# Kernel optimization log

Measured on AMD Instinct MI355X. Metric: run time of the kernel, lower is better.

The kernel has to match this reference:

```python
import jax, jax.numpy as jnp
import numpy as np

B, N = 4096, 64
HID, NHEAD, NLAYERS, OUT = 128, 4, 2, 1
LIDAR, PROC = 20, 20
FOV = 0.35 * np.pi
MAXD = 10.0
LN_EPS = 1e-5


def _lin(x, W, b):
    # torch.nn.Linear: y = x @ W.T + b, W is [out, in]
    return x @ W.T + b


def _ln(x, g, b):
    m = jnp.mean(x, -1, keepdims=True)
    v = jnp.var(x, -1, keepdims=True)  # population variance, as torch LayerNorm
    return (x - m) / jnp.sqrt(v + LN_EPS) * g + b


def _adj_mask(pos):
    # pos: [B,N,2]. Edge i -> j exists where final_mask[b,i,j] (src=i, dst=j).
    dx = pos[:, :, 0][:, :, None] - pos[:, :, 0][:, None, :]  # x_i - x_j
    dy = pos[:, :, 1][:, :, None] - pos[:, :, 1][:, None, :]
    dist = jnp.sqrt(dx * dx + dy * dy)
    ang = jnp.arctan2(dy, dx)
    ang = (ang + np.pi) % (2 * np.pi) - np.pi
    eye = jnp.eye(pos.shape[1], dtype=bool)
    return (~eye)[None] & (jnp.abs(ang) <= FOV) & (dist <= MAXD)


def _forward(data, W_l1, b_l1, W_l2, b_l2, W11, b11, W12, b12, W21, b21, W22, b22,
             Wqkv, bqkv, Wo, bo, ln1_g, ln1_b, Wf1, bf1, Wf2, bf2, ln2_g, ln2_b, Wfc, bfc):
    orig, lidar = data[..., :7], data[..., 7:]
    lf = jax.nn.relu(_lin(jax.nn.relu(_lin(lidar, W_l1, b_l1)), W_l2, b_l2))
    x = jnp.concatenate([orig, lf], -1)  # [B,N,PROC+7]
    # graph construction is index/mask logic -> no gradient through it
    m = jax.lax.stop_gradient(_adj_mask(x[..., :2])).astype(x.dtype)  # [B,N,N]
    # GINConv (eps=0): h_j = nn(x_j + sum_{i: i->j} x_i)
    aggr = jnp.einsum('bij,bif->bjf', m, x)
    h = jax.nn.relu(_lin(jax.nn.relu(_lin(x + aggr, W11, b11)), W12, b12))
    aggr = jnp.einsum('bij,bif->bjf', m, h)
    h = jax.nn.relu(_lin(jax.nn.relu(_lin(h + aggr, W21, b21)), W22, b22))
    # TransformerEncoder over x.unsqueeze(1): seq_len == 1 per node, so the
    # softmax over a single key is exactly 1 -> attn(x) = out_proj(v_proj(x)).
    t = h.reshape(B * N, HID)
    for l in range(NLAYERS):
        Wv, bv = Wqkv[l][2 * HID:], bqkv[l][2 * HID:]
        attn = _lin(_lin(t, Wv, bv), Wo[l], bo[l])
        t = _ln(t + attn, ln1_g[l], ln1_b[l])
        ff = _lin(jax.nn.relu(_lin(t, Wf1[l], bf1[l])), Wf2[l], bf2[l])
        t = _ln(t + ff, ln2_g[l], ln2_b[l])
    return _lin(t.reshape(B, N, HID), Wfc, bfc)  # [B,N,OUT]


def setup_inputs():
    key = jax.random.key(0)
    ks = iter(jax.random.split(key, 40))
    def p(shape, s=0.05):
        return jax.random.normal(next(ks), shape, jnp.float32) * s
    return dict(
        data=jax.random.normal(next(ks), (B, N, 7 + LIDAR), jnp.float32),
        W_l1=p((HID, LIDAR)), b_l1=p((HID,)),
        W_l2=p((PROC, HID)), b_l2=p((PROC,)),
        W11=p((HID, PROC + 7)), b11=p((HID,)),
        W12=p((HID, HID)), b12=p((HID,)),
        W21=p((HID, HID)), b21=p((HID,)),
        W22=p((HID, HID)), b22=p((HID,)),
        Wqkv=p((NLAYERS, 3 * HID, HID)), bqkv=p((NLAYERS, 3 * HID)),
        Wo=p((NLAYERS, HID, HID)), bo=p((NLAYERS, HID)),
        ln1_g=jnp.ones((NLAYERS, HID), jnp.float32), ln1_b=jnp.zeros((NLAYERS, HID), jnp.float32),
        Wf1=p((NLAYERS, HID, HID)), bf1=p((NLAYERS, HID)),
        Wf2=p((NLAYERS, HID, HID)), bf2=p((NLAYERS, HID)),
        ln2_g=jnp.ones((NLAYERS, HID), jnp.float32), ln2_b=jnp.zeros((NLAYERS, HID), jnp.float32),
        Wfc=p((OUT, HID)), bfc=p((OUT,)),
    )


def reference(data, W_l1, b_l1, W_l2, b_l2, W11, b11, W12, b12, W21, b21, W22, b22,
              Wqkv, bqkv, Wo, bo, ln1_g, ln1_b, Wf1, bf1, Wf2, bf2, ln2_g, ln2_b, Wfc, bfc):
    return _forward(data, W_l1, b_l1, W_l2, b_l2, W11, b11, W12, b12, W21, b21, W22, b22,
                    Wqkv, bqkv, Wo, bo, ln1_g, ln1_b, Wf1, bf1, Wf2, bf2, ln2_g, ln2_b, Wfc, bfc)
```

## Files before the change

kernel.cpp:

```cpp
#include <hip/hip_runtime.h>
#include <math.h>

#define NB 4096
#define NN 64

typedef _Float16 h8 __attribute__((ext_vector_type(8)));
typedef _Float16 h4 __attribute__((ext_vector_type(4)));
typedef float f4 __attribute__((ext_vector_type(4)));
typedef unsigned long long u64;

typedef const __attribute__((address_space(1))) void* gas_t;
typedef __attribute__((address_space(3))) void* las_t;

__device__ __forceinline__ void gload16(const void* g, void* l) {
  __builtin_amdgcn_global_load_lds((gas_t)g, (las_t)l, 16, 0, 0);
}
__device__ __forceinline__ void rbar() {
  asm volatile("" ::: "memory");
  __builtin_amdgcn_s_barrier();
  asm volatile("" ::: "memory");
}
__device__ __forceinline__ void lgkm0() {
  asm volatile("s_waitcnt lgkmcnt(0)" ::: "memory");
}
template<int N> __device__ __forceinline__ void waitv() {
  if constexpr (N == 0) asm volatile("s_waitcnt vmcnt(0)" ::: "memory");
  else                  asm volatile("s_waitcnt vmcnt(1)" ::: "memory");
  __builtin_amdgcn_sched_barrier(0);
}

__device__ __forceinline__ int aoff(int row, int colb) {
  return row * 256 + (colb ^ ((row & 7) << 4));
}
__device__ __forceinline__ h8 ald8(const char* a, int row, int colb) {
  return *(const h8*)(a + aoff(row, colb));
}
__device__ __forceinline__ void ast8(char* a, int row, int colb, h8 v) {
  *(h8*)(a + aoff(row, colb)) = v;
}
__device__ __forceinline__ _Float16 ald(const char* a, int row, int colb) {
  return *(const _Float16*)(a + aoff(row, colb));
}
__device__ __forceinline__ void ast(char* a, int row, int colb, _Float16 v) {
  *(_Float16*)(a + aoff(row, colb)) = v;
}

__global__ void prepA(
    const float* __restrict__ W_l1, const float* __restrict__ W_l2,
    const float* __restrict__ W11, const float* __restrict__ W12,
    const float* __restrict__ W21, const float* __restrict__ W22,
    const float* __restrict__ Wf1, const float* __restrict__ Wf2,
    const float* __restrict__ b_l1, const float* __restrict__ b_l2,
    const float* __restrict__ b11, const float* __restrict__ b12,
    const float* __restrict__ b21, const float* __restrict__ b22,
    const float* __restrict__ bf1, const float* __restrict__ bf2,
    const float* __restrict__ ln1_g, const float* __restrict__ ln1_b,
    const float* __restrict__ ln2_g, const float* __restrict__ ln2_b,
    _Float16* __restrict__ ws)
{
  const int e = blockIdx.x * 256 + threadIdx.x;
  float v;
  if (e < 4096) { const int o = e >> 5, k = e & 31; v = (k < 20) ? W_l1[o * 20 + k] : 0.f; }
  else if (e < 8192) { const int i = e - 4096; const int o = i >> 7, k = i & 127; v = (o < 20) ? W_l2[o * 128 + k] : 0.f; }
  else if (e < 12288) { const int i = e - 8192; const int o = i >> 5, k = i & 31; v = (k < 27) ? W11[o * 27 + k] : 0.f; }
  else if (e < 28672) v = W12[e - 12288];
  else if (e < 45056) v = W21[e - 28672];
  else if (e < 61440) v = W22[e - 45056];
  else if (e < 94208) return;
  else if (e < 126976) v = Wf1[e - 94208];
  else if (e < 159744) v = Wf2[e - 126976];
  else {
    const int p = e - 159744;
    if (p >= 2560) return;
    const int idx = p >> 7, col = p & 127;
    switch (idx) {
      case 0: v = b_l1[col]; break;
      case 1: v = (col < 20) ? b_l2[col] : 0.f; break;
      case 2: v = b11[col]; break;
      case 3: v = b12[col]; break;
      case 4: v = b21[col]; break;
      case 5: v = b22[col]; break;
      case 8: v = bf1[col]; break;
      case 9: v = bf2[col]; break;
      case 10: v = bf1[128 + col]; break;
      case 11: v = bf2[128 + col]; break;
      case 12: v = ln1_g[col]; break;
      case 13: v = ln1_b[col]; break;
      case 14: v = ln2_g[col]; break;
      case 15: v = ln2_b[col]; break;
      case 16: v = ln1_g[128 + col]; break;
      case 17: v = ln1_b[128 + col]; break;
      case 18: v = ln2_g[128 + col]; break;
      case 19: v = ln2_b[128 + col]; break;
      default: v = 0.f; break;
    }
  }
  ws[e] = (_Float16)v;
}

__global__ void prepB(
    const float* __restrict__ Wqkv, const float* __restrict__ bqkv,
    const float* __restrict__ Wo, const float* __restrict__ bo,
    _Float16* __restrict__ ws)
{
  if (blockIdx.x < 128) {
    const int e = blockIdx.x * 256 + threadIdx.x;
    const int l = e >> 14, r = e & 16383, o = r >> 7, k = r & 127;
    const float* wo = Wo + (l * 128 + o) * 128;
    const float* wv = Wqkv + l * 49152 + 32768 + k;
    float acc = 0.f;
#pragma unroll 4
    for (int m = 0; m < 128; ++m) acc += wo[m] * wv[m * 128];
    ws[61440 + e] = (_Float16)acc;
  } else {
    const int t = threadIdx.x;
    const int l = t >> 7, o = t & 127;
    const float* wo = Wo + (l * 128 + o) * 128;
    const float* bv = bqkv + l * 384 + 256;
    float acc = bo[l * 128 + o];
    for (int m = 0; m < 128; ++m) acc += bv[m] * wo[m];
    ws[159744 + (6 + l) * 128 + o] = (_Float16)acc;
  }
}

__device__ __forceinline__ void stage64(const _Float16* __restrict__ Wp, int KT,
                                        int kc, int oc, char* buf, int tid) {
  const int o = tid >> 2, kq = tid & 3;
  const int kreal = kq ^ ((o >> 1) & 3);
  gload16(Wp + (oc * 64 + o) * KT + kc * 32 + kreal * 8, buf + tid * 16);
}
__device__ __forceinline__ void stage32(const _Float16* __restrict__ Wp,
                                        int kc, char* buf, int tid) {
  const int o = tid >> 3, u = tid & 7;
  const int ureal = u ^ (o & 7);
  gload16(Wp + o * 128 + kc * 64 + ureal * 8, buf + tid * 16);
}

struct Cap { h4 q0[8]; h4 q1[8]; };

template<int EPI, bool CAP, bool LAST, typename PF>
__device__ __forceinline__ Cap mm128_stage(
    const _Float16* __restrict__ Wp, char* g0, char* g1,
    const _Float16* pb, int bidx, Cap rin,
    char* wbase, int q0, int tid, PF&& pf)
{
  const int lane = tid & 63, wv = tid >> 6, lc = lane & 15, kg = lane >> 4;
  const int nrow = wv * 16 + lc;

  h8 bf0[4], bf1[4];
#pragma unroll
  for (int i = 0; i < 4; ++i) {
    bf0[i] = ald8(g0, nrow, i * 64 + kg * 16);
    bf1[i] = ald8(g1, nrow, i * 64 + kg * 16);
  }
  Cap rout{};
#pragma unroll
  for (int oc = 0; oc < 2; ++oc) {
    f4 a0[4], a1[4];
#pragma unroll
    for (int t = 0; t < 4; ++t) { a0[t] = (f4){0.f,0.f,0.f,0.f}; a1[t] = (f4){0.f,0.f,0.f,0.f}; }
#pragma unroll
    for (int kc = 0; kc < 4; ++kc) {
      const int ql = oc * 4 + kc;
      if (LAST && ql == 7) waitv<0>(); else waitv<1>();
      rbar();
      const int s = ql + 2;
      char* nbuf = wbase + ((q0 + s) % 3) * 4096;
      if (s < 8) stage64(Wp, 128, s & 3, s >> 2, nbuf, tid);
      else pf(s - 8, nbuf);
      const char* wb = wbase + ((q0 + ql) % 3) * 4096;
#pragma unroll
      for (int t = 0; t < 4; ++t) {
        const int o = t * 16 + lc;
        const int kq = kg ^ ((o >> 1) & 3);
        const h8 af = *(const h8*)(wb + (o * 4 + kq) * 16);
        a0[t] = __builtin_amdgcn_mfma_f32_16x16x32_f16(af, bf0[kc], a0[t], 0, 0, 0);
        a1[t] = __builtin_amdgcn_mfma_f32_16x16x32_f16(af, bf1[kc], a1[t], 0, 0, 0);
      }
    }
#pragma unroll
    for (int t = 0; t < 4; ++t) {
      const int slot = oc * 4 + t;
      const int fb = slot * 16 + kg * 4;
      const int cb = fb * 2;
      h4 bq{};
      if constexpr (EPI != 1) bq = *(const h4*)(pb + bidx * 128 + fb);
      h4 r0q{}, r1q{};
      if constexpr (EPI == 2) {
        r0q = *(const h4*)(g0 + aoff(nrow, cb));
        r1q = *(const h4*)(g1 + aoff(nrow, cb));
      }
      if constexpr (CAP) {
        rout.q0[slot] = *(const h4*)(g0 + aoff(nrow, cb));
        rout.q1[slot] = *(const h4*)(g1 + aoff(nrow, cb));
      }
      h4 o0, o1;
#pragma unroll
      for (int r = 0; r < 4; ++r) {
        float v0 = a0[t][r], v1 = a1[t][r];
        if constexpr (EPI != 1) { v0 += (float)bq[r]; v1 += (float)bq[r]; }
        if constexpr (EPI == 2) { v0 += (float)r0q[r]; v1 += (float)r1q[r]; }
        if constexpr (EPI == 3) { v0 += (float)rin.q0[slot][r]; v1 += (float)rin.q1[slot][r]; }
        if constexpr (EPI == 0) { v0 = fmaxf(v0, 0.f); v1 = fmaxf(v1, 0.f); }
        o0[r] = (_Float16)v0; o1[r] = (_Float16)v1;
      }
      *(h4*)(g0 + aoff(nrow, cb)) = o0;
      *(h4*)(g1 + aoff(nrow, cb)) = o1;
    }
  }
  return rout;
}

template<typename PF>
__device__ __forceinline__ void mm32z_stage(
    const _Float16* __restrict__ Wp, char* g0, char* g1,
    char* wbase, int q0, int tid, PF&& pf)
{
  const int lane = tid & 63, wv = tid >> 6, lc = lane & 15, kg = lane >> 4;
  const int nrow = wv * 16 + lc;
  const h8 bf0 = ald8(g0, nrow, 64 + kg * 16);
  const h8 bf1 = ald8(g1, nrow, 64 + kg * 16);
#pragma unroll
  for (int oc = 0; oc < 2; ++oc) {
    waitv<1>(); rbar();
    pf(oc, wbase + ((q0 + oc + 2) % 3) * 4096);
    const char* wb = wbase + ((q0 + oc) % 3) * 4096;
    f4 a0[4], a1[4];
#pragma unroll
    for (int t = 0; t < 4; ++t) { a0[t] = (f4){0.f,0.f,0.f,0.f}; a1[t] = (f4){0.f,0.f,0.f,0.f}; }
#pragma unroll
    for (int t = 0; t < 4; ++t) {
      const int o = t * 16 + lc;
      const int kq = kg ^ ((o >> 1) & 3);
      const h8 af = *(const h8*)(wb + (o * 4 + kq) * 16);
      a0[t] = __builtin_amdgcn_mfma_f32_16x16x32_f16(af, bf0, a0[t], 0, 0, 0);
      a1[t] = __builtin_amdgcn_mfma_f32_16x16x32_f16(af, bf1, a1[t], 0, 0, 0);
    }
#pragma unroll
    for (int t = 0; t < 4; ++t) {
      const int fb = (oc * 4 + t) * 16 + kg * 4;
      const int cb = fb * 2;
      h4 o0, o1;
#pragma unroll
      for (int r = 0; r < 4; ++r) { o0[r] = (_Float16)a0[t][r]; o1[r] = (_Float16)a1[t][r]; }
      *(h4*)(g0 + aoff(nrow, cb)) = o0;
      *(h4*)(g1 + aoff(nrow, cb)) = o1;
    }
  }
}

__device__ __forceinline__ void agg_ip(const u64* mc, char* G, const _Float16* pb,
                                       int bidx, int tid)
{
  const int lane = tid & 63, wv = tid >> 6, lc = lane & 15, kg = lane >> 4;
  const int c0 = wv * 32 + lc;
  u64 mrow[4];
#pragma unroll
  for (int rt = 0; rt < 4; ++rt) mrow[rt] = mc[rt * 16 + lc];
  h8 bf[2][2];
#pragma unroll
  for (int ks = 0; ks < 2; ++ks)
#pragma unroll
    for (int ct = 0; ct < 2; ++ct)
#pragma unroll
      for (int e = 0; e < 8; ++e)
        bf[ks][ct][e] = ald(G, ks * 32 + kg * 8 + e, (c0 + ct * 16) * 2);
  lgkm0(); rbar();
  f4 acc[4][2];
#pragma unroll
  for (int rt = 0; rt < 4; ++rt) { acc[rt][0] = (f4){0.f,0.f,0.f,0.f}; acc[rt][1] = (f4){0.f,0.f,0.f,0.f}; }
#pragma unroll
  for (int ks = 0; ks < 2; ++ks)
#pragma unroll
    for (int rt = 0; rt < 4; ++rt) {
      const unsigned int byte = (unsigned int)(mrow[rt] >> (ks * 32 + kg * 8)) & 0xffu;
      h8 af;
#pragma unroll
      for (int e = 0; e < 8; ++e) af[e] = (_Float16)((byte >> e) & 1u);
#pragma unroll
      for (int ct = 0; ct < 2; ++ct)
        acc[rt][ct] = __builtin_amdgcn_mfma_f32_16x16x32_f16(af, bf[ks][ct], acc[rt][ct], 0, 0, 0);
    }
#pragma unroll
  for (int ct = 0; ct < 2; ++ct) {
    const int col = c0 + ct * 16;
    const float bv = (float)pb[bidx * 128 + col];
#pragma unroll
    for (int rt = 0; rt < 4; ++rt)
#pragma unroll
      for (int qq = 0; qq < 4; ++qq)
        ast(G, rt * 16 + kg * 4 + qq, col * 2, (_Float16)fmaxf(acc[rt][ct][qq] + bv, 0.f));
  }
}

__device__ __forceinline__ void layer_norm(char* buf, const _Float16* pb, int lnidx, int tid)
{
  const int n = tid >> 2, q = tid & 3;
  float vals[32];
#pragma unroll
  for (int u = 0; u < 4; ++u) {
    const h8 v = ald8(buf, n, q * 64 + u * 16);
#pragma unroll
    for (int e = 0; e < 8; ++e) vals[u * 8 + e] = (float)v[e];
  }
  float s = 0.f;
#pragma unroll
  for (int u = 0; u < 32; ++u) s += vals[u];
  s += __shfl_xor(s, 1, 64);
  s += __shfl_xor(s, 2, 64);
  const float mean = s * 0.0078125f;
  float vv = 0.f;
#pragma unroll
  for (int u = 0; u < 32; ++u) { const float d = vals[u] - mean; vv = fmaf(d, d, vv); }
  vv += __shfl_xor(vv, 1, 64);
  vv += __shfl_xor(vv, 2, 64);
  const float rstd = 1.0f / sqrtf(vv * 0.0078125f + 1e-5f);
#pragma unroll
  for (int u = 0; u < 4; ++u) {
    h8 o;
#pragma unroll
    for (int e = 0; e < 8; ++e) {
      const int col = q * 32 + u * 8 + e;
      const float gg = (float)pb[lnidx * 128 + col];
      const float bb = (float)pb[(lnidx + 1) * 128 + col];
      o[e] = (_Float16)((vals[u * 8 + e] - mean) * rstd * gg + bb);
    }
    ast8(buf, n, q * 64 + u * 16, o);
  }
}

struct SM {
  alignas(16) char G0[16384];
  alignas(16) char G1[16384];
  alignas(16) char WB[12288];
  alignas(16) char PB[5120];
  u64 mcol[2][64];
};

__global__ __launch_bounds__(256, 2)
void gin_critic_kernel(
    const float* __restrict__ data,
    const float* __restrict__ Wfc, const float* __restrict__ bfc,
    const _Float16* __restrict__ ws,
    float* __restrict__ out)
{
  __shared__ SM sm;
  const int tid = threadIdx.x;
  const int lane = tid & 63, wv = tid >> 6, lc = lane & 15, kg = lane >> 4;
  const int row0 = wv * 16 + lc, rb = wv * 16 + kg * 4;
  const int b = blockIdx.x;
  const long base = (long)b * 2 * NN * 27;
  char* G0 = sm.G0; char* G1 = sm.G1; char* wbase = sm.WB;
  const _Float16* pb = (const _Float16*)sm.PB;

  const _Float16* Wl1p = ws + 0;
  const _Float16* Wl2p = ws + 4096;
  const _Float16* W11p = ws + 8192;
  const _Float16* W12p = ws + 12288;
  const _Float16* W21p = ws + 28672;
  const _Float16* W22p = ws + 45056;
  const _Float16* Wat0 = ws + 61440;
  const _Float16* Wat1 = ws + 61440 + 16384;
  const _Float16* Wf1_0 = ws + 94208;
  const _Float16* Wf1_1 = ws + 94208 + 16384;
  const _Float16* Wf2_0 = ws + 126976;
  const _Float16* Wf2_1 = ws + 126976 + 16384;

#pragma unroll
  for (int i = 0; i < 14; ++i) {
    const int idx = tid + i * 256;
    const int cidx = idx < 3456 ? idx : 3455;
    float v = data[base + cidx];
    asm volatile("" : "+v"(v));
    if (idx < 3456) {
      const int gi = idx / 1728;
      const int r = idx - gi * 1728;
      const int n = r / 27, f = r - n * 27;
      char* Gg = gi ? G1 : G0;
      if (f < 7) ast(Gg, n, 64 + f * 2, (_Float16)v);
      else       ast(Gg, n, (f - 7) * 2, (_Float16)v);
    }
  }
  if (tid < 128) {
    const int gi = tid >> 6, n = tid & 63;
    char* Gg = gi ? G1 : G0;
#pragma unroll
    for (int c = 20; c < 32; ++c) ast(Gg, n, c * 2, (_Float16)0.f);
#pragma unroll
    for (int c = 59; c < 64; ++c) ast(Gg, n, c * 2, (_Float16)0.f);
  }
  const float* pp = data + base + (long)(wv >> 1) * 1728 + lane * 27;
  const float px = pp[0], py = pp[1];
  lgkm0(); rbar();

  {
    const int g = wv >> 1;
    const float FOVF = (float)(0.35 * 3.14159265358979323846);
    const double TT = tan(0.35 * 3.14159265358979323846);
    const double T2 = TT * TT;
    for (int jj = 0; jj < 32; ++jj) {
      const int j = (wv & 1) * 32 + jj;
      const float x0j = __shfl(px, j, 64);
      const float x1j = __shfl(py, j, 64);
      const float dxf = px - x0j;
      const float dyf = py - x1j;
      const float dist = sqrtf(dxf * dxf + dyf * dyf);
      bool pred;
      if (lane == j || dist > 10.0f) {
        pred = false;
      } else if (dxf <= 0.0f) {
        pred = (dxf == 0.0f && dyf == 0.0f);
      } else {
        const double qa = (double)dyf * (double)dyf;
        const double qb = (double)dxf * (double)dxf * T2;
        if (qa <= qb * 0.99999) pred = true;
        else if (qa >= qb * 1.00001) pred = false;
        else pred = (fabsf((float)atan2((double)dyf, (double)dxf)) <= FOVF);
      }
      const u64 bal = __ballot(pred);
      if (lane == 0) sm.mcol[g][j] = bal | (1ull << j);
    }
  }

  gload16(ws + 159744 + (size_t)tid * 8, sm.PB + (size_t)tid * 16);
  gload16(ws + 159744 + 2048 + (size_t)(tid & 63) * 8, sm.PB + 4096 + (size_t)(tid & 63) * 16);
  stage64(Wl1p, 32, 0, 0, wbase + 0 * 4096, tid);
  stage32(Wl2p, 0, wbase + 1 * 4096, tid);

  h8 axl0, axl1;
  f4 l20[2], l21[2];
  l20[0] = l20[1] = l21[0] = l21[1] = (f4){0.f,0.f,0.f,0.f};
  waitv<1>(); rbar();
  stage64(Wl1p, 32, 0, 1, wbase + 2 * 4096, tid);
  axl0 = ald8(G0, row0, kg * 16);
  axl1 = ald8(G1, row0, kg * 16);
  {
    const char* wb = wbase + 0 * 4096;
    f4 a0[4], a1[4];
#pragma unroll
    for (int t = 0; t < 4; ++t) { a0[t] = (f4){0.f,0.f,0.f,0.f}; a1[t] = (f4){0.f,0.f,0.f,0.f}; }
#pragma unroll
    for (int t = 0; t < 4; ++t) {
      const int o = t * 16 + lc;
      const int kq = kg ^ ((o >> 1) & 3);
      const h8 bf = *(const h8*)(wb + (o * 4 + kq) * 16);
      a0[t] = __builtin_amdgcn_mfma_f32_16x16x32_f16(axl0, bf, a0[t], 0, 0, 0);
      a1[t] = __builtin_amdgcn_mfma_f32_16x16x32_f16(axl1, bf, a1[t], 0, 0, 0);
    }
#pragma unroll
    for (int t = 0; t < 4; ++t) {
      const int col = t * 16 + lc;
      const float bv = (float)pb[0 * 128 + col];
#pragma unroll
      for (int r = 0; r < 4; ++r) {
        ast(G0, rb + r, 128 + col * 2, (_Float16)fmaxf(a0[t][r] + bv, 0.f));
        ast(G1, rb + r, 128 + col * 2, (_Float16)fmaxf(a1[t][r] + bv, 0.f));
      }
    }
  }
  waitv<1>(); rbar();
  stage32(Wl2p, 1, wbase + 0 * 4096, tid);
  {
    const char* wb = wbase + 1 * 4096;
    h8 ah0[2], ah1[2];
#pragma unroll
    for (int i = 0; i < 2; ++i) {
      ah0[i] = ald8(G0, row0, 128 + i * 64 + kg * 16);
      ah1[i] = ald8(G1, row0, 128 + i * 64 + kg * 16);
    }
#pragma unroll
    for (int ks = 0; ks < 2; ++ks)
#pragma unroll
      for (int ct = 0; ct < 2; ++ct) {
        const int o = ct * 16 + lc;
        const int u = (ks * 4 + kg) ^ (o & 7);
        const h8 bf = *(const h8*)(wb + (o * 8 + u) * 16);
        l20[ct] = __builtin_amdgcn_mfma_f32_16x16x32_f16(ah0[ks], bf, l20[ct], 0, 0, 0);
        l21[ct] = __builtin_amdgcn_mfma_f32_16x16x32_f16(ah1[ks], bf, l21[ct], 0, 0, 0);
      }
  }
  waitv<1>(); rbar();
  stage64(W11p, 32, 0, 0, wbase + 1 * 4096, tid);
  {
    const char* wb = wbase + 2 * 4096;
    f4 a0[4], a1[4];
#pragma unroll
    for (int t = 0; t < 4; ++t) { a0[t] = (f4){0.f,0.f,0.f,0.f}; a1[t] = (f4){0.f,0.f,0.f,0.f}; }
#pragma unroll
    for (int t = 0; t < 4; ++t) {
      const int o = t * 16 + lc;
      const int kq = kg ^ ((o >> 1) & 3);
      const h8 bf = *(const h8*)(wb + (o * 4 + kq) * 16);
      a0[t] = __builtin_amdgcn_mfma_f32_16x16x32_f16(axl0, bf, a0[t], 0, 0, 0);
      a1[t] = __builtin_amdgcn_mfma_f32_16x16x32_f16(axl1, bf, a1[t], 0, 0, 0);
    }
#pragma unroll
    for (int t = 0; t < 4; ++t) {
      const int col = t * 16 + lc;
      const float bv = (float)pb[0 * 128 + 64 + col];
#pragma unroll
      for (int r = 0; r < 4; ++r) {
        ast(G0, rb + r, 128 + col * 2, (_Float16)fmaxf(a0[t][r] + bv, 0.f));
        ast(G1, rb + r, 128 + col * 2, (_Float16)fmaxf(a1[t][r] + bv, 0.f));
      }
    }
  }
  waitv<1>(); rbar();
  stage64(W11p, 32, 0, 1, wbase + 2 * 4096, tid);
  {
    const char* wb = wbase + 0 * 4096;
    h8 ah0[2], ah1[2];
#pragma unroll
    for (int i = 0; i < 2; ++i) {
      ah0[i] = ald8(G0, row0, 128 + i * 64 + kg * 16);
      ah1[i] = ald8(G1, row0, 128 + i * 64 + kg * 16);
    }
#pragma unroll
    for (int ks = 0; ks < 2; ++ks)
#pragma unroll
      for (int ct = 0; ct < 2; ++ct) {
        const int o = ct * 16 + lc;
        const int u = (ks * 4 + kg) ^ (o & 7);
        const h8 bf = *(const h8*)(wb + (o * 8 + u) * 16);
        l20[ct] = __builtin_amdgcn_mfma_f32_16x16x32_f16(ah0[ks], bf, l20[ct], 0, 0, 0);
        l21[ct] = __builtin_amdgcn_mfma_f32_16x16x32_f16(ah1[ks], bf, l21[ct], 0, 0, 0);
      }
#pragma unroll
    for (int ct = 0; ct < 2; ++ct) {
      const int col = ct * 16 + lc;
      if (col < 20) {
        const float bv = (float)pb[1 * 128 + col];
#pragma unroll
        for (int r = 0; r < 4; ++r) {
          ast(G0, rb + r, 78 + col * 2, (_Float16)fmaxf(l20[ct][r] + bv, 0.f));
          ast(G1, rb + r, 78 + col * 2, (_Float16)fmaxf(l21[ct][r] + bv, 0.f));
        }
      }
    }
  }

  Cap rz{};
  mm32z_stage(W11p, G0, G1, wbase, 4, tid,
      [&](int s, char* buf) { stage64(W12p, 128, s, 0, buf, tid); });
  lgkm0(); rbar();
  agg_ip(sm.mcol[0], G0, pb, 2, tid);
  agg_ip(sm.mcol[1], G1, pb, 2, tid);
  lgkm0(); rbar();
  mm128_stage<0, false, false>(W12p, G0, G1, pb, 3, rz, wbase, 6, tid,
      [&](int s, char* buf) { stage64(W21p, 128, s, 0, buf, tid); });
  mm128_stage<1, false, false>(W21p, G0, G1, pb, 0, rz, wbase, 14, tid,
      [&](int s, char* buf) { stage64(W22p, 128, s, 0, buf, tid); });
  lgkm0(); rbar();
  agg_ip(sm.mcol[0], G0, pb, 4, tid);
  agg_ip(sm.mcol[1], G1, pb, 4, tid);
  lgkm0(); rbar();
  mm128_stage<0, false, false>(W22p, G0, G1, pb, 5, rz, wbase, 22, tid,
      [&](int s, char* buf) { stage64(Wat0, 128, s, 0, buf, tid); });
  mm128_stage<2, false, false>(Wat0, G0, G1, pb, 6, rz, wbase, 30, tid,
      [&](int s, char* buf) { stage64(Wf1_0, 128, s, 0, buf, tid); });
  layer_norm(G0, pb, 12, tid);
  layer_norm(G1, pb, 12, tid);
  Cap c0 = mm128_stage<0, true, false>(Wf1_0, G0, G1, pb, 8, rz, wbase, 38, tid,
      [&](int s, char* buf) { stage64(Wf2_0, 128, s, 0, buf, tid); });
  mm128_stage<3, false, false>(Wf2_0, G0, G1, pb, 9, c0, wbase, 46, tid,
      [&](int s, char* buf) { stage64(Wat1, 128, s, 0, buf, tid); });
  layer_norm(G0, pb, 14, tid);
  layer_norm(G1, pb, 14, tid);
  mm128_stage<2, false, false>(Wat1, G0, G1, pb, 7, rz, wbase, 54, tid,
      [&](int s, char* buf) { stage64(Wf1_1, 128, s, 0, buf, tid); });
  layer_norm(G0, pb, 16, tid);
  layer_norm(G1, pb, 16, tid);
  Cap c1 = mm128_stage<0, true, false>(Wf1_1, G0, G1, pb, 10, rz, wbase, 62, tid,
      [&](int s, char* buf) { stage64(Wf2_1, 128, s, 0, buf, tid); });
  mm128_stage<3, false, true>(Wf2_1, G0, G1, pb, 11, c1, wbase, 70, tid,
      [&](int, char*) {});
  layer_norm(G0, pb, 18, tid);
  layer_norm(G1, pb, 18, tid);

#pragma unroll
  for (int g = 0; g < 2; ++g) {
    const char* Pg = g ? G1 : G0;
    const int n = tid >> 2, q = tid & 3;
    float s = 0.f;
#pragma unroll
    for (int u = 0; u < 4; ++u) {
      const h8 v = ald8(Pg, n, q * 64 + u * 16);
      const float4 w0 = *(const float4*)(Wfc + q * 32 + u * 8);
      const float4 w1 = *(const float4*)(Wfc + q * 32 + u * 8 + 4);
      s = fmaf((float)v[0], w0.x, s); s = fmaf((float)v[1], w0.y, s);
      s = fmaf((float)v[2], w0.z, s); s = fmaf((float)v[3], w0.w, s);
      s = fmaf((float)v[4], w1.x, s); s = fmaf((float)v[5], w1.y, s);
      s = fmaf((float)v[6], w1.z, s); s = fmaf((float)v[7], w1.w, s);
    }
    s += __shfl_xor(s, 1, 64);
    s += __shfl_xor(s, 2, 64);
    if (q == 0) out[((long)b * 2 + g) * NN + n] = s + bfc[0];
  }
}

extern "C" void kernel_launch(void* const* d_in, const int* in_sizes, int n_in,
                              void* d_out, int out_size, void* d_ws, size_t ws_size,
                              hipStream_t stream) {
  const float* data  = (const float*)d_in[0];
  const float* W_l1  = (const float*)d_in[1];
  const float* b_l1  = (const float*)d_in[2];
  const float* W_l2  = (const float*)d_in[3];
  const float* b_l2  = (const float*)d_in[4];
  const float* W11   = (const float*)d_in[5];
  const float* b11   = (const float*)d_in[6];
  const float* W12   = (const float*)d_in[7];
  const float* b12   = (const float*)d_in[8];
  const float* W21   = (const float*)d_in[9];
  const float* b21   = (const float*)d_in[10];
  const float* W22   = (const float*)d_in[11];
  const float* b22   = (const float*)d_in[12];
  const float* Wqkv  = (const float*)d_in[13];
  const float* bqkv  = (const float*)d_in[14];
  const float* Wo    = (const float*)d_in[15];
  const float* bo    = (const float*)d_in[16];
  const float* ln1_g = (const float*)d_in[17];
  const float* ln1_b = (const float*)d_in[18];
  const float* Wf1   = (const float*)d_in[19];
  const float* bf1   = (const float*)d_in[20];
  const float* Wf2   = (const float*)d_in[21];
  const float* bf2   = (const float*)d_in[22];
  const float* ln2_g = (const float*)d_in[23];
  const float* ln2_b = (const float*)d_in[24];
  const float* Wfc   = (const float*)d_in[25];
  const float* bfc   = (const float*)d_in[26];

  _Float16* ws = (_Float16*)d_ws;

  prepA<<<dim3(634), dim3(256), 0, stream>>>(
      W_l1, W_l2, W11, W12, W21, W22, Wf1, Wf2,
      b_l1, b_l2, b11, b12, b21, b22, bf1, bf2,
      ln1_g, ln1_b, ln2_g, ln2_b, ws);
  prepB<<<dim3(129), dim3(256), 0, stream>>>(Wqkv, bqkv, Wo, bo, ws);

  gin_critic_kernel<<<dim3(NB / 2), dim3(256), 0, stream>>>(
      data, Wfc, bfc, ws, (float*)d_out);
}
```

Before: 198.8 us.

## Store pre-aggregation GEMM output transposed so adjacency aggregation reads contiguous fragments

```diff
diff --git a/kernel.cpp b/kernel.cpp
--- a/kernel.cpp
+++ b/kernel.cpp
@@ -30,7 +30,7 @@
 }
 
 __device__ __forceinline__ int aoff(int row, int colb) {
-  return row * 256 + (colb ^ ((row & 7) << 4));
+  return row * 256 + (colb ^ ((row & 15) << 4));
 }
 __device__ __forceinline__ h8 ald8(const char* a, int row, int colb) {
   return *(const h8*)(a + aoff(row, colb));
@@ -43,6 +43,9 @@
 }
 __device__ __forceinline__ void ast(char* a, int row, int colb, _Float16 v) {
   *(_Float16*)(a + aoff(row, colb)) = v;
+}
+__device__ __forceinline__ int zoff(int f, int nb) {
+  return f * 128 + ((((nb >> 4) ^ (f & 7)) << 4) | (nb & 15));
 }
 
 __global__ void prepA(
@@ -198,7 +201,7 @@
 #pragma unroll
       for (int r = 0; r < 4; ++r) {
         float v0 = a0[t][r], v1 = a1[t][r];
-        if constexpr (EPI != 1) { v0 += (float)bq[r]; v1 += (float)bq[r]; }
+        v0 += (float)bq[r]; v1 += (float)bq[r];
         if constexpr (EPI == 2) { v0 += (float)r0q[r]; v1 += (float)r1q[r]; }
         if constexpr (EPI == 3) { v0 += (float)rin.q0[slot][r]; v1 += (float)rin.q1[slot][r]; }
         if constexpr (EPI == 0) { v0 = fmaxf(v0, 0.f); v1 = fmaxf(v1, 0.f); }
@@ -212,14 +215,14 @@
 }
 
 template<typename PF>
-__device__ __forceinline__ void mm32z_stage(
+__device__ __forceinline__ void mm32z_old(
     const _Float16* __restrict__ Wp, char* g0, char* g1,
     char* wbase, int q0, int tid, PF&& pf)
 {
   const int lane = tid & 63, wv = tid >> 6, lc = lane & 15, kg = lane >> 4;
-  const int nrow = wv * 16 + lc;
-  const h8 bf0 = ald8(g0, nrow, 64 + kg * 16);
-  const h8 bf1 = ald8(g1, nrow, 64 + kg * 16);
+  const int row0 = wv * 16 + lc, rb = wv * 16 + kg * 4;
+  const h8 af0 = ald8(g0, row0, 64 + kg * 16);
+  const h8 af1 = ald8(g1, row0, 64 + kg * 16);
 #pragma unroll
   for (int oc = 0; oc < 2; ++oc) {
     waitv<1>(); rbar();
@@ -232,64 +235,126 @@
     for (int t = 0; t < 4; ++t) {
       const int o = t * 16 + lc;
       const int kq = kg ^ ((o >> 1) & 3);
-      const h8 af = *(const h8*)(wb + (o * 4 + kq) * 16);
-      a0[t] = __builtin_amdgcn_mfma_f32_16x16x32_f16(af, bf0, a0[t], 0, 0, 0);
-      a1[t] = __builtin_amdgcn_mfma_f32_16x16x32_f16(af, bf1, a1[t], 0, 0, 0);
+      const h8 wf = *(const h8*)(wb + (o * 4 + kq) * 16);
+      a0[t] = __builtin_amdgcn_mfma_f32_16x16x32_f16(af0, wf, a0[t], 0, 0, 0);
+      a1[t] = __builtin_amdgcn_mfma_f32_16x16x32_f16(af1, wf, a1[t], 0, 0, 0);
     }
 #pragma unroll
     for (int t = 0; t < 4; ++t) {
-      const int fb = (oc * 4 + t) * 16 + kg * 4;
-      const int cb = fb * 2;
+      const int o = oc * 64 + t * 16 + lc;
       h4 o0, o1;
 #pragma unroll
       for (int r = 0; r < 4; ++r) { o0[r] = (_Float16)a0[t][r]; o1[r] = (_Float16)a1[t][r]; }
-      *(h4*)(g0 + aoff(nrow, cb)) = o0;
-      *(h4*)(g1 + aoff(nrow, cb)) = o1;
-    }
-  }
-}
-
-__device__ __forceinline__ void agg_ip(const u64* mc, char* G, const _Float16* pb,
-                                       int bidx, int tid)
+      *(h4*)(g0 + zoff(o, rb * 2)) = o0;
+      *(h4*)(g1 + zoff(o, rb * 2)) = o1;
+    }
+  }
+}
+
+template<typename PF>
+__device__ __forceinline__ void mm128z_old(
+    const _Float16* __restrict__ Wp, char* g0, char* g1,
+    char* wbase, int q0, int tid, PF&& pf)
 {
   const int lane = tid & 63, wv = tid >> 6, lc = lane & 15, kg = lane >> 4;
-  const int c0 = wv * 32 + lc;
-  u64 mrow[4];
-#pragma unroll
-  for (int rt = 0; rt < 4; ++rt) mrow[rt] = mc[rt * 16 + lc];
-  h8 bf[2][2];
+  const int row0 = wv * 16 + lc, rb = wv * 16 + kg * 4;
+  h8 af0[4], af1[4];
+#pragma unroll
+  for (int i = 0; i < 4; ++i) {
+    af0[i] = ald8(g0, row0, i * 64 + kg * 16);
+    af1[i] = ald8(g1, row0, i * 64 + kg * 16);
+  }
+#pragma unroll
+  for (int oc = 0; oc < 2; ++oc) {
+    f4 a0[4], a1[4];
+#pragma unroll
+    for (int t = 0; t < 4; ++t) { a0[t] = (f4){0.f,0.f,0.f,0.f}; a1[t] = (f4){0.f,0.f,0.f,0.f}; }
+#pragma unroll
+    for (int kc = 0; kc < 4; ++kc) {
+      const int ql = oc * 4 + kc;
+      waitv<1>();
+      rbar();
+      const int s = ql + 2;
+      char* nbuf = wbase + ((q0 + s) % 3) * 4096;
+      if (s < 8) stage64(Wp, 128, s & 3, s >> 2, nbuf, tid);
+      else pf(s - 8, nbuf);
+      const char* wb = wbase + ((q0 + ql) % 3) * 4096;
+#pragma unroll
+      for (int t = 0; t < 4; ++t) {
+        const int o = t * 16 + lc;
+        const int kq = kg ^ ((o >> 1) & 3);
+        const h8 wf = *(const h8*)(wb + (o * 4 + kq) * 16);
+        a0[t] = __builtin_amdgcn_mfma_f32_16x16x32_f16(af0[kc], wf, a0[t], 0, 0, 0);
+        a1[t] = __builtin_amdgcn_mfma_f32_16x16x32_f16(af1[kc], wf, a1[t], 0, 0, 0);
+      }
+    }
+#pragma unroll
+    for (int t = 0; t < 4; ++t) {
+      const int o = oc * 64 + t * 16 + lc;
+      h4 o0, o1;
+#pragma unroll
+      for (int r = 0; r < 4; ++r) { o0[r] = (_Float16)a0[t][r]; o1[r] = (_Float16)a1[t][r]; }
+      *(h4*)(g0 + zoff(o, rb * 2)) = o0;
+      *(h4*)(g1 + zoff(o, rb * 2)) = o1;
+    }
+  }
+}
+
+__device__ __forceinline__ void agg2_zt(
+    const u64* mc0, const u64* mc1, char* g0, char* g1,
+    const _Float16* pb, int bidx, int tid)
+{
+  const int lane = tid & 63, wv = tid >> 6, lc = lane & 15, kg = lane >> 4;
+  const int fb = wv * 32;
+  h8 a0[2][2], a1[2][2];
+#pragma unroll
+  for (int mt = 0; mt < 2; ++mt)
+#pragma unroll
+    for (int ks = 0; ks < 2; ++ks) {
+      a0[mt][ks] = *(const h8*)(g0 + zoff(fb + mt * 16 + lc, ks * 64 + kg * 16));
+      a1[mt][ks] = *(const h8*)(g1 + zoff(fb + mt * 16 + lc, ks * 64 + kg * 16));
+    }
+  u64 mr0[4], mr1[4];
+#pragma unroll
+  for (int nt = 0; nt < 4; ++nt) { mr0[nt] = mc0[nt * 16 + lc]; mr1[nt] = mc1[nt * 16 + lc]; }
+  lgkm0(); rbar();
+  f4 c0[2][4], c1[2][4];
+#pragma unroll
+  for (int mt = 0; mt < 2; ++mt)
+#pragma unroll
+    for (int nt = 0; nt < 4; ++nt) { c0[mt][nt] = (f4){0.f,0.f,0.f,0.f}; c1[mt][nt] = (f4){0.f,0.f,0.f,0.f}; }
 #pragma unroll
   for (int ks = 0; ks < 2; ++ks)
 #pragma unroll
-    for (int ct = 0; ct < 2; ++ct)
-#pragma unroll
-      for (int e = 0; e < 8; ++e)
-        bf[ks][ct][e] = ald(G, ks * 32 + kg * 8 + e, (c0 + ct * 16) * 2);
-  lgkm0(); rbar();
-  f4 acc[4][2];
-#pragma unroll
-  for (int rt = 0; rt < 4; ++rt) { acc[rt][0] = (f4){0.f,0.f,0.f,0.f}; acc[rt][1] = (f4){0.f,0.f,0.f,0.f}; }
-#pragma unroll
-  for (int ks = 0; ks < 2; ++ks)
-#pragma unroll
-    for (int rt = 0; rt < 4; ++rt) {
-      const unsigned int byte = (unsigned int)(mrow[rt] >> (ks * 32 + kg * 8)) & 0xffu;
-      h8 af;
-#pragma unroll
-      for (int e = 0; e < 8; ++e) af[e] = (_Float16)((byte >> e) & 1u);
-#pragma unroll
-      for (int ct = 0; ct < 2; ++ct)
-        acc[rt][ct] = __builtin_amdgcn_mfma_f32_16x16x32_f16(af, bf[ks][ct], acc[rt][ct], 0, 0, 0);
-    }
-#pragma unroll
-  for (int ct = 0; ct < 2; ++ct) {
-    const int col = c0 + ct * 16;
-    const float bv = (float)pb[bidx * 128 + col];
-#pragma unroll
-    for (int rt = 0; rt < 4; ++rt)
-#pragma unroll
-      for (int qq = 0; qq < 4; ++qq)
-        ast(G, rt * 16 + kg * 4 + qq, col * 2, (_Float16)fmaxf(acc[rt][ct][qq] + bv, 0.f));
+    for (int nt = 0; nt < 4; ++nt) {
+      h8 b0, b1;
+#pragma unroll
+      for (int e = 0; e < 8; ++e) {
+        b0[e] = (_Float16)((mr0[nt] >> (ks * 32 + kg * 8 + e)) & 1ull);
+        b1[e] = (_Float16)((mr1[nt] >> (ks * 32 + kg * 8 + e)) & 1ull);
+      }
+#pragma unroll
+      for (int mt = 0; mt < 2; ++mt) {
+        c0[mt][nt] = __builtin_amdgcn_mfma_f32_16x16x32_f16(a0[mt][ks], b0, c0[mt][nt], 0, 0, 0);
+        c1[mt][nt] = __builtin_amdgcn_mfma_f32_16x16x32_f16(a1[mt][ks], b1, c1[mt][nt], 0, 0, 0);
+      }
+    }
+#pragma unroll
+  for (int mt = 0; mt < 2; ++mt) {
+    const int f0 = fb + mt * 16 + kg * 4;
+    const h4 bq = *(const h4*)(pb + bidx * 128 + f0);
+#pragma unroll
+    for (int nt = 0; nt < 4; ++nt) {
+      const int j = nt * 16 + lc;
+      h4 o0, o1;
+#pragma unroll
+      for (int r = 0; r < 4; ++r) {
+        o0[r] = (_Float16)fmaxf(c0[mt][nt][r] + (float)bq[r], 0.f);
+        o1[r] = (_Float16)fmaxf(c1[mt][nt][r] + (float)bq[r], 0.f);
+      }
+      *(h4*)(g0 + aoff(j, f0 * 2)) = o0;
+      *(h4*)(g1 + aoff(j, f0 * 2)) = o1;
+    }
   }
 }
 
@@ -540,19 +605,17 @@
   }
 
   Cap rz{};
-  mm32z_stage(W11p, G0, G1, wbase, 4, tid,
+  mm32z_old(W11p, G0, G1, wbase, 4, tid,
       [&](int s, char* buf) { stage64(W12p, 128, s, 0, buf, tid); });
   lgkm0(); rbar();
-  agg_ip(sm.mcol[0], G0, pb, 2, tid);
-  agg_ip(sm.mcol[1], G1, pb, 2, tid);
+  agg2_zt(sm.mcol[0], sm.mcol[1], G0, G1, pb, 2, tid);
   lgkm0(); rbar();
   mm128_stage<0, false, false>(W12p, G0, G1, pb, 3, rz, wbase, 6, tid,
       [&](int s, char* buf) { stage64(W21p, 128, s, 0, buf, tid); });
-  mm128_stage<1, false, false>(W21p, G0, G1, pb, 0, rz, wbase, 14, tid,
+  mm128z_old(W21p, G0, G1, wbase, 14, tid,
       [&](int s, char* buf) { stage64(W22p, 128, s, 0, buf, tid); });
   lgkm0(); rbar();
-  agg_ip(sm.mcol[0], G0, pb, 4, tid);
-  agg_ip(sm.mcol[1], G1, pb, 4, tid);
+  agg2_zt(sm.mcol[0], sm.mcol[1], G0, G1, pb, 4, tid);
   lgkm0(); rbar();
   mm128_stage<0, false, false>(W22p, G0, G1, pb, 5, rz, wbase, 22, tid,
       [&](int s, char* buf) { stage64(Wat0, 128, s, 0, buf, tid); });
```

Result: faster. 193.3 us (-2.7%).
